# Kernel optimization log

Measured on AMD Instinct MI355X. Metric: run time of the kernel, lower is better.

Reference implementation:

```python
import jax, jax.numpy as jnp
import numpy as np

N = 2048   # num_points
D = 16     # dims: points are DxD complex symmetric matrices (upper half space)
B = 32     # batch of input point ids
EPS = 1e-6


def _siegel_dist(z1, z2):
    """Siegel upper-half-space distance between batches of points.

    z1, z2: [P, 2, D, D] real-stacked complex symmetric matrices (real, imag),
    imag part SPD. Returns [P] distances.
    """
    X1, Y1 = z1[:, 0], z1[:, 1]
    X2, Y2 = z2[:, 0], z2[:, 1]
    # Y2^{-1/2} via eigh (Y2 is SPD)
    w, U = jnp.linalg.eigh(Y2)
    inv_sqrt = jnp.einsum('pij,pj,pkj->pik', U, 1.0 / jnp.sqrt(jnp.maximum(w, 1e-8)), U)
    # isometry sending z2 -> i*Id:  Z3 = Y2^{-1/2} (Z1 - X2) Y2^{-1/2}
    Zc = (X1 - X2) + 1j * Y1                      # complex64 [P, D, D]
    S = inv_sqrt.astype(Zc.dtype)
    Z3 = S @ Zc @ S
    iI = 1j * jnp.eye(D, dtype=Zc.dtype)
    # Cayley map to bounded domain: W = (Z3 - iI)(Z3 + iI)^{-1}; both factors symmetric,
    # so A B^{-1} = (B^{-1} A)^T and we can use a single batched solve.
    W = jnp.swapaxes(jnp.linalg.solve(Z3 + iI, Z3 - iI), -1, -2)
    # singular values of (symmetric) W via eigvalsh of W^H W
    ev = jnp.linalg.eigvalsh(jnp.conj(jnp.swapaxes(W, -1, -2)) @ W)
    s = jnp.sqrt(jnp.clip(ev, EPS, (1.0 - EPS) ** 2))   # s in (0, 1)
    v = jnp.log((1.0 + s) / (1.0 - s))
    return jnp.sqrt(jnp.sum(v * v, axis=-1))


def setup_inputs() -> dict:
    rng = np.random.default_rng(0)
    # valid upper-half points: symmetric real part, SPD imaginary part
    X = rng.normal(size=(N, D, D)).astype(np.float32) * 0.1
    X = 0.5 * (X + X.transpose(0, 2, 1))
    A = rng.normal(size=(N, D, D)).astype(np.float32) * 0.1
    Y = A @ A.transpose(0, 2, 1) + np.eye(D, dtype=np.float32)
    embeds = np.stack([X, Y], axis=1)                    # [N, 2, D, D]
    graph_distances = rng.random((N, N)).astype(np.float32) * 9.0 + 1.0
    # host-side expansion of get_src_and_dst_from_seq for input_index = arange(B)
    src, dst = [], []
    for a in range(B):
        for b in range(a + 1, N):
            src.append(a)
            dst.append(b)
    return {
        'embeds': jnp.asarray(embeds),
        'graph_distances': jnp.asarray(graph_distances),
        'src': jnp.asarray(np.asarray(src, np.int64)),
        'dst': jnp.asarray(np.asarray(dst, np.int64)),
    }


def reference(embeds, graph_distances, src, dst):
    md = _siegel_dist(embeds[src], embeds[dst])          # [P]
    gd = graph_distances[src, dst]                       # [P]
    loss = jnp.abs((md / gd) ** 2 - 1.0)
    return jnp.sum(loss)
```

## Files before the change

kernel.cpp:

```cpp
#include <hip/hip_runtime.h>
#include <math.h>

#define NPTS 2048
#define LDM 17
#define MAXSWEEP 8
#define NS_ITERS 9
#define SWZ(i,j) (((i)<<4) + ((((i)+(j))&15)))

__device__ __forceinline__ void wave_sync(){
    asm volatile("s_waitcnt lgkmcnt(0)" ::: "memory");
    __builtin_amdgcn_sched_barrier(0);
}

__device__ __forceinline__ void matmul16(const float* A, const float* B, float* C, int lane){
    int i  = lane & 15;
    int j0 = (lane >> 4) * 4;
    float c0 = 0.f, c1 = 0.f, c2 = 0.f, c3 = 0.f;
#pragma unroll
    for (int k = 0; k < 16; ++k){
        float a = A[i*LDM + k];
        c0 = fmaf(a, B[k*LDM + j0 + 0], c0);
        c1 = fmaf(a, B[k*LDM + j0 + 1], c1);
        c2 = fmaf(a, B[k*LDM + j0 + 2], c2);
        c3 = fmaf(a, B[k*LDM + j0 + 3], c3);
    }
    C[i*LDM + j0 + 0] = c0;
    C[i*LDM + j0 + 1] = c1;
    C[i*LDM + j0 + 2] = c2;
    C[i*LDM + j0 + 3] = c3;
}

__device__ __forceinline__ void jp(int r, int k, int& pI, int& qI){
    if (k == 0){ pI = r; qI = 15; }
    else {
        int a = r + k;      if (a >= 15) a -= 15;
        int b = r + 15 - k; if (b >= 15) b -= 15;
        pI = a < b ? a : b;
        qI = a < b ? b : a;
    }
}

__global__ __launch_bounds__(256) void precompute_invsqrt(const float* __restrict__ embeds,
                                                          float* __restrict__ Sout){
    __shared__ float buf[4][5][16*LDM];
    const int w    = threadIdx.x >> 6;
    const int lane = threadIdx.x & 63;
    const int n    = blockIdx.x * 4 + w;

    float* Bm = buf[w][0];
    float* Zm = buf[w][1];
    float* Tm = buf[w][2];
    float* B2 = buf[w][3];
    float* Z2 = buf[w][4];

    const float* gY = embeds + (size_t)n * 512 + 256;

    float ss = 0.f;
#pragma unroll
    for (int t = 0; t < 4; ++t){
        int e = lane + t*64;
        float v = gY[e];
        Bm[(e >> 4)*LDM + (e & 15)] = v;
        ss += v*v;
    }
#pragma unroll
    for (int m = 1; m < 64; m <<= 1) ss += __shfl_xor(ss, m);
    float f    = sqrtf(ss);
    float invf = 1.0f / f;
    __syncthreads();

#pragma unroll
    for (int t = 0; t < 4; ++t){
        int e = lane + t*64; int i = e >> 4, j = e & 15;
        Bm[i*LDM + j] *= invf;
        Zm[i*LDM + j]  = (i == j) ? 1.f : 0.f;
    }
    __syncthreads();

    for (int it = 0; it < NS_ITERS; ++it){
        matmul16(Zm, Bm, Tm, lane);
        __syncthreads();
#pragma unroll
        for (int t = 0; t < 4; ++t){
            int e = lane + t*64; int i = e >> 4, j = e & 15;
            float v = -0.5f * Tm[i*LDM + j] + ((i == j) ? 1.5f : 0.f);
            Tm[i*LDM + j] = v;
        }
        __syncthreads();
        matmul16(Bm, Tm, B2, lane);
        matmul16(Tm, Zm, Z2, lane);
        __syncthreads();
        float* tp;
        tp = Bm; Bm = B2; B2 = tp;
        tp = Zm; Zm = Z2; Z2 = tp;
    }

    float sc = rsqrtf(f);
    float* out = Sout + (size_t)n * 256;
#pragma unroll
    for (int t = 0; t < 4; ++t){
        int e = lane + t*64; int i = e >> 4, j = e & 15;
        out[e] = Zm[i*LDM + j] * sc;
    }
}

__global__ __launch_bounds__(256) void siegel_pairs(const float* __restrict__ embeds,
                                                    const float* __restrict__ gdist,
                                                    const int*   __restrict__ src,
                                                    const int*   __restrict__ dst,
                                                    const float* __restrict__ S,
                                                    float* __restrict__ partials,
                                                    int P){
    __shared__ float  buf[4][4][16*LDM];
    __shared__ float4 rotv[4][8];
    __shared__ float  wterm[4];

    const int w    = threadIdx.x >> 6;
    const int lane = threadIdx.x & 63;

    const int p = blockIdx.x * 4 + w;
    const bool valid = (p < P);
    const int pp = valid ? p : 0;
    const int a = src[pp];
    const int b = dst[pp];

    float* M0 = buf[w][0];
    float* M1 = buf[w][1];
    float* M2 = buf[w][2];
    float* M3 = buf[w][3];
    float2* CRCI = (float2*)M1;

    const float* e1 = embeds + (size_t)a * 512;
    const float* e2 = embeds + (size_t)b * 512;
    const float* S2 = S + (size_t)b * 256;

#pragma unroll
    for (int t = 0; t < 4; ++t){
        int e = lane + t*64; int i = e >> 4, j = e & 15;
        M0[i*LDM + j] = S2[e];
        M1[i*LDM + j] = e1[e] - e2[e];
        M2[i*LDM + j] = e1[256 + e];
    }
    wave_sync();

    matmul16(M0, M1, M3, lane);
    wave_sync();
    matmul16(M3, M0, M1, lane);
    wave_sync();
    matmul16(M0, M2, M3, lane);
    wave_sync();
    matmul16(M3, M0, M2, lane);
    wave_sync();

    {
        int i = lane & 15, j0 = (lane >> 4) * 4;
        float g0=0,g1=0,g2=0,g3=0, q0=0,q1=0,q2=0,q3=0;
#pragma unroll
        for (int k = 0; k < 16; ++k){
            float x = M1[i*LDM + k];
            float y = M2[i*LDM + k];
            float xk0 = M1[k*LDM + j0+0], yk0 = M2[k*LDM + j0+0];
            float xk1 = M1[k*LDM + j0+1], yk1 = M2[k*LDM + j0+1];
            float xk2 = M1[k*LDM + j0+2], yk2 = M2[k*LDM + j0+2];
            float xk3 = M1[k*LDM + j0+3], yk3 = M2[k*LDM + j0+3];
            g0 += x*xk0 + y*yk0;  q0 += y*xk0 - x*yk0;
            g1 += x*xk1 + y*yk1;  q1 += y*xk1 - x*yk1;
            g2 += x*xk2 + y*yk2;  q2 += y*xk2 - x*yk2;
            g3 += x*xk3 + y*yk3;  q3 += y*xk3 - x*yk3;
        }
        M3[i*LDM + j0+0] = g0 + ((i == j0+0) ? 1.f : 0.f);
        M3[i*LDM + j0+1] = g1 + ((i == j0+1) ? 1.f : 0.f);
        M3[i*LDM + j0+2] = g2 + ((i == j0+2) ? 1.f : 0.f);
        M3[i*LDM + j0+3] = g3 + ((i == j0+3) ? 1.f : 0.f);
        M0[i*LDM + j0+0] = q0;
        M0[i*LDM + j0+1] = q1;
        M0[i*LDM + j0+2] = q2;
        M0[i*LDM + j0+3] = q3;
    }
    wave_sync();

    for (int k = 0; k < 16; ++k){
        float akk = M2[k*LDM + k];
        float rs  = rsqrtf(akk);
        if (lane == 0) M2[k*LDM + k] = rs;
        if (lane > k && lane < 16) M2[lane*LDM + k] *= rs;
        wave_sync();
        int i = lane & 15, jg = lane >> 4;
        if (i > k){
            float lik = M2[i*LDM + k];
            for (int j = k + 1 + jg; j <= i; j += 4)
                M2[i*LDM + j] -= lik * M2[j*LDM + k];
        }
        wave_sync();
    }

    {
        float* Mb = (lane < 16) ? M3 : ((lane < 32) ? M0 : (float*)0);
        int col = lane & 15;
        if (Mb){
            float z[16];
#pragma unroll
            for (int i = 0; i < 16; ++i){
                float v = Mb[i*LDM + col];
#pragma unroll
                for (int m = 0; m < i; ++m) v -= M2[i*LDM + m] * z[m];
                z[i] = v * M2[i*LDM + i];
            }
#pragma unroll
            for (int i = 0; i < 16; ++i) Mb[i*LDM + col] = z[i];
        }
    }
    wave_sync();

    {
        float* Mb = (lane < 16) ? M3 : ((lane < 32) ? M0 : (float*)0);
        int r = lane & 15;
        if (Mb){
            float z[16];
#pragma unroll
            for (int j = 0; j < 16; ++j){
                float v = Mb[r*LDM + j];
#pragma unroll
                for (int m = 0; m < j; ++m) v -= M2[j*LDM + m] * z[m];
                z[j] = v * M2[j*LDM + j];
            }
#pragma unroll
            for (int j = 0; j < 16; ++j) Mb[r*LDM + j] = z[j];
        }
    }
    wave_sync();

    {
        int i = lane & 15, jg = lane >> 4;
#pragma unroll
        for (int t = 0; t < 4; ++t){
            int j = jg + 4*t;
            float cr = 0.5f*(M3[i*LDM + j] + M3[j*LDM + i]);
            float ci = 0.5f*(M0[i*LDM + j] - M0[j*LDM + i]);
            CRCI[SWZ(i,j)] = make_float2(cr, ci);
        }
    }
    wave_sync();

    const int k1 = lane >> 3, k2 = lane & 7;
    const bool isdiag = (k1 == k2);
    unsigned qa[15];
#pragma unroll
    for (int r = 0; r < 15; ++r){
        int p1,q1,p2,q2;
        jp(r, k1, p1, q1);
        jp(r, k2, p2, q2);
        qa[r] = (unsigned)SWZ(p1,p2) | ((unsigned)SWZ(p1,q2) << 8)
              | ((unsigned)SWZ(q1,p2) << 16) | ((unsigned)SWZ(q1,q2) << 24);
    }

#pragma unroll 1
    for (int sweep = 0; sweep < MAXSWEEP; ++sweep){
#pragma unroll
        for (int r = 0; r < 15; ++r){
            unsigned q = qa[r];
            int iPP = q & 255, iPQ = (q >> 8) & 255, iQP = (q >> 16) & 255, iQQ = q >> 24;
            if (isdiag){
                float app = CRCI[iPP].x;
                float aqq = CRCI[iQQ].x;
                float2 bb = CRCI[iPQ];
                float n2 = bb.x*bb.x + bb.y*bb.y;
                float dd = 0.5f*(aqq - app);
                float h  = sqrtf(fmaf(dd, dd, n2));
                float den = fabsf(dd) + h + 1e-38f;
                float g  = 1.0f/den;
                g = (dd < 0.f) ? -g : g;
                float tt = (n2*g)*g;
                float c  = rsqrtf(1.f + tt);
                float cg = c*g;
                rotv[w][k1] = make_float4(c, cg*bb.x, cg*bb.y, 0.f);
            }
            wave_sync();

            float4 r1 = rotv[w][k1];
            float4 r2 = rotv[w][k2];
            float2 a00 = CRCI[iPP], a01 = CRCI[iPQ];
            float2 a10 = CRCI[iQP], a11 = CRCI[iQQ];

            float t0x = r1.y*a10.x - r1.z*a10.y, t0y = r1.y*a10.y + r1.z*a10.x;
            float t1x = r1.y*a11.x - r1.z*a11.y, t1y = r1.y*a11.y + r1.z*a11.x;
            float u0x = r1.y*a00.x + r1.z*a00.y, u0y = r1.y*a00.y - r1.z*a00.x;
            float u1x = r1.y*a01.x + r1.z*a01.y, u1y = r1.y*a01.y - r1.z*a01.x;
            float b00x = fmaf(r1.x, a00.x, -t0x), b00y = fmaf(r1.x, a00.y, -t0y);
            float b01x = fmaf(r1.x, a01.x, -t1x), b01y = fmaf(r1.x, a01.y, -t1y);
            float b10x = fmaf(r1.x, a10.x,  u0x), b10y = fmaf(r1.x, a10.y,  u0y);
            float b11x = fmaf(r1.x, a11.x,  u1x), b11y = fmaf(r1.x, a11.y,  u1y);

            float v0x = r2.y*b01x + r2.z*b01y, v0y = r2.y*b01y - r2.z*b01x;
            float w0x = r2.y*b00x - r2.z*b00y, w0y = r2.y*b00y + r2.z*b00x;
            float v1x = r2.y*b11x + r2.z*b11y, v1y = r2.y*b11y - r2.z*b11x;
            float w1x = r2.y*b10x - r2.z*b10y, w1y = r2.y*b10y + r2.z*b10x;
            CRCI[iPP] = make_float2(fmaf(r2.x, b00x, -v0x), fmaf(r2.x, b00y, -v0y));
            CRCI[iPQ] = make_float2(fmaf(r2.x, b01x,  w0x), fmaf(r2.x, b01y,  w0y));
            CRCI[iQP] = make_float2(fmaf(r2.x, b10x, -v1x), fmaf(r2.x, b10y, -v1y));
            CRCI[iQQ] = make_float2(fmaf(r2.x, b11x,  w1x), fmaf(r2.x, b11y,  w1y));
            wave_sync();
        }

        if (sweep >= 2 && sweep < MAXSWEEP-1){
            float o2 = 0.f, s2 = 0.f;
#pragma unroll
            for (int t = 0; t < 4; ++t){
                int e = lane + t*64; int i = e >> 4, j = e & 15;
                float2 v = CRCI[SWZ(i,j)];
                float m = v.x*v.x + v.y*v.y;
                s2 += m;
                if (i != j) o2 += m;
            }
#pragma unroll
            for (int m = 1; m < 64; m <<= 1){
                o2 += __shfl_xor(o2, m);
                s2 += __shfl_xor(s2, m);
            }
            if (o2 <= 1.6e-11f * s2) break;
        }
    }

    float t2 = 0.f;
    if (lane < 16){
        float mu  = CRCI[SWZ(lane,lane)].x;
        float lam = (mu - 2.f) / (mu + 2.f);
        const float lo = 1e-6f;
        const float hi = (1.f - 1e-6f) * (1.f - 1e-6f);
        lam = fminf(fmaxf(lam, lo), hi);
        float sv = sqrtf(lam);
        float v  = logf((1.f + sv) / (1.f - sv));
        t2 = v * v;
    }
#pragma unroll
    for (int m = 1; m < 16; m <<= 1) t2 += __shfl_xor(t2, m);
    if (lane == 0){
        float gd   = gdist[(size_t)a * NPTS + b];
        float term = fabsf(t2 / (gd * gd) - 1.f);
        wterm[w] = valid ? term : 0.f;
    }
    __syncthreads();
    if (threadIdx.x == 0)
        partials[blockIdx.x] = wterm[0] + wterm[1] + wterm[2] + wterm[3];
}

__global__ __launch_bounds__(256) void reduce_partials(const float* __restrict__ partials,
                                                       int n, float* __restrict__ out){
    __shared__ double sd[256];
    double s = 0.0;
    for (int i = threadIdx.x; i < n; i += 256) s += (double)partials[i];
    sd[threadIdx.x] = s;
    __syncthreads();
    for (int st = 128; st > 0; st >>= 1){
        if (threadIdx.x < st) sd[threadIdx.x] += sd[threadIdx.x + st];
        __syncthreads();
    }
    if (threadIdx.x == 0) out[0] = (float)sd[0];
}

extern "C" void kernel_launch(void* const* d_in, const int* in_sizes, int n_in,
                              void* d_out, int out_size, void* d_ws, size_t ws_size,
                              hipStream_t stream){
    const float* embeds = (const float*)d_in[0];
    const float* gdist  = (const float*)d_in[1];
    const int*   src    = (const int*)d_in[2];
    const int*   dst    = (const int*)d_in[3];
    const int P = in_sizes[2];

    float* S        = (float*)d_ws;
    float* partials = S + (size_t)NPTS * 256;

    const int nb = (P + 3) / 4;

    precompute_invsqrt<<<dim3(NPTS/4), dim3(256), 0, stream>>>(embeds, S);
    siegel_pairs<<<dim3(nb), dim3(256), 0, stream>>>(embeds, gdist, src, dst, S, partials, P);
    reduce_partials<<<dim3(1), dim3(256), 0, stream>>>(partials, nb, (float*)d_out);
}
```

Baseline: 1.205 ms.

## Vectorize LDS accesses and pass Jacobi rotations via shuffles instead of LDS

Pads the LDS row stride to 20 so rows are 16-byte aligned, and uses float4 loads and stores for the matmuls, the Gram product and the global-to-LDS staging. In the Jacobi sweep, each rotation step now reads its 2x2 block once and broadcasts rotation parameters through __shfl instead of writing them to LDS, which removes one wave_sync per step. The convergence check reuses the norms of each lane's final updated block rather than rescanning the matrix. The padding raises LDS use, and the shuffles add cross-lane traffic in exchange.

```diff
diff --git a/kernel.cpp b/kernel.cpp
--- a/kernel.cpp
+++ b/kernel.cpp
@@ -2,7 +2,7 @@
 #include <math.h>
 
 #define NPTS 2048
-#define LDM 17
+#define LDM 20
 #define MAXSWEEP 8
 #define NS_ITERS 9
 #define SWZ(i,j) (((i)<<4) + ((((i)+(j))&15)))
@@ -19,15 +19,13 @@
 #pragma unroll
     for (int k = 0; k < 16; ++k){
         float a = A[i*LDM + k];
-        c0 = fmaf(a, B[k*LDM + j0 + 0], c0);
-        c1 = fmaf(a, B[k*LDM + j0 + 1], c1);
-        c2 = fmaf(a, B[k*LDM + j0 + 2], c2);
-        c3 = fmaf(a, B[k*LDM + j0 + 3], c3);
-    }
-    C[i*LDM + j0 + 0] = c0;
-    C[i*LDM + j0 + 1] = c1;
-    C[i*LDM + j0 + 2] = c2;
-    C[i*LDM + j0 + 3] = c3;
+        float4 b = *reinterpret_cast<const float4*>(&B[k*LDM + j0]);
+        c0 = fmaf(a, b.x, c0);
+        c1 = fmaf(a, b.y, c1);
+        c2 = fmaf(a, b.z, c2);
+        c3 = fmaf(a, b.w, c3);
+    }
+    *reinterpret_cast<float4*>(&C[i*LDM + j0]) = make_float4(c0, c1, c2, c3);
 }
 
 __device__ __forceinline__ void jp(int r, int k, int& pI, int& qI){
@@ -42,7 +40,7 @@
 
 __global__ __launch_bounds__(256) void precompute_invsqrt(const float* __restrict__ embeds,
                                                           float* __restrict__ Sout){
-    __shared__ float buf[4][5][16*LDM];
+    __shared__ __attribute__((aligned(16))) float buf[4][5][16*LDM];
     const int w    = threadIdx.x >> 6;
     const int lane = threadIdx.x & 63;
     const int n    = blockIdx.x * 4 + w;
@@ -111,9 +109,8 @@
                                                     const float* __restrict__ S,
                                                     float* __restrict__ partials,
                                                     int P){
-    __shared__ float  buf[4][4][16*LDM];
-    __shared__ float4 rotv[4][8];
-    __shared__ float  wterm[4];
+    __shared__ __attribute__((aligned(16))) float buf[4][4][16*LDM];
+    __shared__ float wterm[4];
 
     const int w    = threadIdx.x >> 6;
     const int lane = threadIdx.x & 63;
@@ -130,16 +127,20 @@
     float* M3 = buf[w][3];
     float2* CRCI = (float2*)M1;
 
-    const float* e1 = embeds + (size_t)a * 512;
-    const float* e2 = embeds + (size_t)b * 512;
-    const float* S2 = S + (size_t)b * 256;
-
-#pragma unroll
-    for (int t = 0; t < 4; ++t){
-        int e = lane + t*64; int i = e >> 4, j = e & 15;
-        M0[i*LDM + j] = S2[e];
-        M1[i*LDM + j] = e1[e] - e2[e];
-        M2[i*LDM + j] = e1[256 + e];
+    const float4* e1v = reinterpret_cast<const float4*>(embeds + (size_t)a * 512);
+    const float4* e2v = reinterpret_cast<const float4*>(embeds + (size_t)b * 512);
+    const float4* S2v = reinterpret_cast<const float4*>(S + (size_t)b * 256);
+
+    {
+        int row = lane >> 2, c4 = (lane & 3) * 4;
+        float4 sv = S2v[lane];
+        float4 x1 = e1v[lane];
+        float4 x2 = e2v[lane];
+        float4 y1 = e1v[64 + lane];
+        *reinterpret_cast<float4*>(&M0[row*LDM + c4]) = sv;
+        *reinterpret_cast<float4*>(&M1[row*LDM + c4]) =
+            make_float4(x1.x - x2.x, x1.y - x2.y, x1.z - x2.z, x1.w - x2.w);
+        *reinterpret_cast<float4*>(&M2[row*LDM + c4]) = y1;
     }
     wave_sync();
 
@@ -159,23 +160,19 @@
         for (int k = 0; k < 16; ++k){
             float x = M1[i*LDM + k];
             float y = M2[i*LDM + k];
-            float xk0 = M1[k*LDM + j0+0], yk0 = M2[k*LDM + j0+0];
-            float xk1 = M1[k*LDM + j0+1], yk1 = M2[k*LDM + j0+1];
-            float xk2 = M1[k*LDM + j0+2], yk2 = M2[k*LDM + j0+2];
-            float xk3 = M1[k*LDM + j0+3], yk3 = M2[k*LDM + j0+3];
-            g0 += x*xk0 + y*yk0;  q0 += y*xk0 - x*yk0;
-            g1 += x*xk1 + y*yk1;  q1 += y*xk1 - x*yk1;
-            g2 += x*xk2 + y*yk2;  q2 += y*xk2 - x*yk2;
-            g3 += x*xk3 + y*yk3;  q3 += y*xk3 - x*yk3;
-        }
-        M3[i*LDM + j0+0] = g0 + ((i == j0+0) ? 1.f : 0.f);
-        M3[i*LDM + j0+1] = g1 + ((i == j0+1) ? 1.f : 0.f);
-        M3[i*LDM + j0+2] = g2 + ((i == j0+2) ? 1.f : 0.f);
-        M3[i*LDM + j0+3] = g3 + ((i == j0+3) ? 1.f : 0.f);
-        M0[i*LDM + j0+0] = q0;
-        M0[i*LDM + j0+1] = q1;
-        M0[i*LDM + j0+2] = q2;
-        M0[i*LDM + j0+3] = q3;
+            float4 xk = *reinterpret_cast<const float4*>(&M1[k*LDM + j0]);
+            float4 yk = *reinterpret_cast<const float4*>(&M2[k*LDM + j0]);
+            g0 += x*xk.x + y*yk.x;  q0 += y*xk.x - x*yk.x;
+            g1 += x*xk.y + y*yk.y;  q1 += y*xk.y - x*yk.y;
+            g2 += x*xk.z + y*yk.z;  q2 += y*xk.z - x*yk.z;
+            g3 += x*xk.w + y*yk.w;  q3 += y*xk.w - x*yk.w;
+        }
+        *reinterpret_cast<float4*>(&M3[i*LDM + j0]) = make_float4(
+            g0 + ((i == j0+0) ? 1.f : 0.f),
+            g1 + ((i == j0+1) ? 1.f : 0.f),
+            g2 + ((i == j0+2) ? 1.f : 0.f),
+            g3 + ((i == j0+3) ? 1.f : 0.f));
+        *reinterpret_cast<float4*>(&M0[i*LDM + j0]) = make_float4(q0, q1, q2, q3);
     }
     wave_sync();
 
@@ -244,6 +241,7 @@
 
     const int k1 = lane >> 3, k2 = lane & 7;
     const bool isdiag = (k1 == k2);
+    const int d1 = 9*k1, d2 = 9*k2;
     unsigned qa[15];
 #pragma unroll
     for (int r = 0; r < 15; ++r){
@@ -254,64 +252,67 @@
               | ((unsigned)SWZ(q1,p2) << 16) | ((unsigned)SWZ(q1,q2) << 24);
     }
 
+    float off2 = 0.f, tot2 = 0.f;
 #pragma unroll 1
     for (int sweep = 0; sweep < MAXSWEEP; ++sweep){
 #pragma unroll
         for (int r = 0; r < 15; ++r){
             unsigned q = qa[r];
             int iPP = q & 255, iPQ = (q >> 8) & 255, iQP = (q >> 16) & 255, iQQ = q >> 24;
+            float2 a00 = CRCI[iPP], a01 = CRCI[iPQ];
+            float2 a10 = CRCI[iQP], a11 = CRCI[iQQ];
+
+            float rc = 1.f, rsx = 0.f, rsy = 0.f;
             if (isdiag){
-                float app = CRCI[iPP].x;
-                float aqq = CRCI[iQQ].x;
-                float2 bb = CRCI[iPQ];
-                float n2 = bb.x*bb.x + bb.y*bb.y;
-                float dd = 0.5f*(aqq - app);
+                float n2 = a01.x*a01.x + a01.y*a01.y;
+                float dd = 0.5f*(a11.x - a00.x);
                 float h  = sqrtf(fmaf(dd, dd, n2));
                 float den = fabsf(dd) + h + 1e-38f;
                 float g  = 1.0f/den;
                 g = (dd < 0.f) ? -g : g;
                 float tt = (n2*g)*g;
-                float c  = rsqrtf(1.f + tt);
-                float cg = c*g;
-                rotv[w][k1] = make_float4(c, cg*bb.x, cg*bb.y, 0.f);
+                rc  = rsqrtf(1.f + tt);
+                float cg = rc*g;
+                rsx = cg*a01.x; rsy = cg*a01.y;
+            }
+            float r1x = __shfl(rc, d1), r1y = __shfl(rsx, d1), r1z = __shfl(rsy, d1);
+            float r2x = __shfl(rc, d2), r2y = __shfl(rsx, d2), r2z = __shfl(rsy, d2);
+
+            float t0x = r1y*a10.x - r1z*a10.y, t0y = r1y*a10.y + r1z*a10.x;
+            float t1x = r1y*a11.x - r1z*a11.y, t1y = r1y*a11.y + r1z*a11.x;
+            float u0x = r1y*a00.x + r1z*a00.y, u0y = r1y*a00.y - r1z*a00.x;
+            float u1x = r1y*a01.x + r1z*a01.y, u1y = r1y*a01.y - r1z*a01.x;
+            float b00x = fmaf(r1x, a00.x, -t0x), b00y = fmaf(r1x, a00.y, -t0y);
+            float b01x = fmaf(r1x, a01.x, -t1x), b01y = fmaf(r1x, a01.y, -t1y);
+            float b10x = fmaf(r1x, a10.x,  u0x), b10y = fmaf(r1x, a10.y,  u0y);
+            float b11x = fmaf(r1x, a11.x,  u1x), b11y = fmaf(r1x, a11.y,  u1y);
+
+            float v0x = r2y*b01x + r2z*b01y, v0y = r2y*b01y - r2z*b01x;
+            float w0x = r2y*b00x - r2z*b00y, w0y = r2y*b00y + r2z*b00x;
+            float v1x = r2y*b11x + r2z*b11y, v1y = r2y*b11y - r2z*b11x;
+            float w1x = r2y*b10x - r2z*b10y, w1y = r2y*b10y + r2z*b10x;
+            float n00x = fmaf(r2x, b00x, -v0x), n00y = fmaf(r2x, b00y, -v0y);
+            float n01x = fmaf(r2x, b01x,  w0x), n01y = fmaf(r2x, b01y,  w0y);
+            float n10x = fmaf(r2x, b10x, -v1x), n10y = fmaf(r2x, b10y, -v1y);
+            float n11x = fmaf(r2x, b11x,  w1x), n11y = fmaf(r2x, b11y,  w1y);
+            CRCI[iPP] = make_float2(n00x, n00y);
+            CRCI[iPQ] = make_float2(n01x, n01y);
+            CRCI[iQP] = make_float2(n10x, n10y);
+            CRCI[iQQ] = make_float2(n11x, n11y);
+
+            if (r == 14){
+                float mPP = n00x*n00x + n00y*n00y;
+                float mPQ = n01x*n01x + n01y*n01y;
+                float mQP = n10x*n10x + n10y*n10y;
+                float mQQ = n11x*n11x + n11y*n11y;
+                tot2 = mPP + mPQ + mQP + mQQ;
+                off2 = isdiag ? (mPQ + mQP) : tot2;
             }
             wave_sync();
-
-            float4 r1 = rotv[w][k1];
-            float4 r2 = rotv[w][k2];
-            float2 a00 = CRCI[iPP], a01 = CRCI[iPQ];
-            float2 a10 = CRCI[iQP], a11 = CRCI[iQQ];
-
-            float t0x = r1.y*a10.x - r1.z*a10.y, t0y = r1.y*a10.y + r1.z*a10.x;
-            float t1x = r1.y*a11.x - r1.z*a11.y, t1y = r1.y*a11.y + r1.z*a11.x;
-            float u0x = r1.y*a00.x + r1.z*a00.y, u0y = r1.y*a00.y - r1.z*a00.x;
-            float u1x = r1.y*a01.x + r1.z*a01.y, u1y = r1.y*a01.y - r1.z*a01.x;
-            float b00x = fmaf(r1.x, a00.x, -t0x), b00y = fmaf(r1.x, a00.y, -t0y);
-            float b01x = fmaf(r1.x, a01.x, -t1x), b01y = fmaf(r1.x, a01.y, -t1y);
-            float b10x = fmaf(r1.x, a10.x,  u0x), b10y = fmaf(r1.x, a10.y,  u0y);
-            float b11x = fmaf(r1.x, a11.x,  u1x), b11y = fmaf(r1.x, a11.y,  u1y);
-
-            float v0x = r2.y*b01x + r2.z*b01y, v0y = r2.y*b01y - r2.z*b01x;
-            float w0x = r2.y*b00x - r2.z*b00y, w0y = r2.y*b00y + r2.z*b00x;
-            float v1x = r2.y*b11x + r2.z*b11y, v1y = r2.y*b11y - r2.z*b11x;
-            float w1x = r2.y*b10x - r2.z*b10y, w1y = r2.y*b10y + r2.z*b10x;
-            CRCI[iPP] = make_float2(fmaf(r2.x, b00x, -v0x), fmaf(r2.x, b00y, -v0y));
-            CRCI[iPQ] = make_float2(fmaf(r2.x, b01x,  w0x), fmaf(r2.x, b01y,  w0y));
-            CRCI[iQP] = make_float2(fmaf(r2.x, b10x, -v1x), fmaf(r2.x, b10y, -v1y));
-            CRCI[iQQ] = make_float2(fmaf(r2.x, b11x,  w1x), fmaf(r2.x, b11y,  w1y));
-            wave_sync();
         }
 
         if (sweep >= 2 && sweep < MAXSWEEP-1){
-            float o2 = 0.f, s2 = 0.f;
-#pragma unroll
-            for (int t = 0; t < 4; ++t){
-                int e = lane + t*64; int i = e >> 4, j = e & 15;
-                float2 v = CRCI[SWZ(i,j)];
-                float m = v.x*v.x + v.y*v.y;
-                s2 += m;
-                if (i != j) o2 += m;
-            }
+            float o2 = off2, s2 = tot2;
 #pragma unroll
             for (int m = 1; m < 64; m <<= 1){
                 o2 += __shfl_xor(o2, m);
@@ -320,6 +321,7 @@
             if (o2 <= 1.6e-11f * s2) break;
         }
     }
+    wave_sync();
 
     float t2 = 0.f;
     if (lane < 16){
```

Result: faster. 1.120 ms (-7.0%).
